# Optimization experiments

Hardware: AMD Instinct MI355X
Metric: run time of the kernel (lower is better)

Reference implementation:

```python
import jax, jax.numpy as jnp
import numpy as np

N_HEAD = 16
NUM_EXPERTS = 8
TOP_K = 2
LN_EPS = 1e-5


def setup_inputs() -> dict:
    key = jax.random.key(0)
    B, T, D = 8, 1024, 1024
    H = 4 * D
    E = NUM_EXPERTS
    ks = jax.random.split(key, 24)
    s = 0.02
    inp = {
        "x": jax.random.normal(ks[0], (B, T, D), jnp.float32),
        "ln1_g": jnp.ones((D,), jnp.float32),
        "ln1_b": jnp.zeros((D,), jnp.float32),
        "ln2_g": jnp.ones((D,), jnp.float32),
        "ln2_b": jnp.zeros((D,), jnp.float32),
        "Wq": jax.random.normal(ks[1], (D, D), jnp.float32) * s,
        "bq": jnp.zeros((D,), jnp.float32),
        "Wk": jax.random.normal(ks[2], (D, D), jnp.float32) * s,
        "bk": jnp.zeros((D,), jnp.float32),
        "Wv": jax.random.normal(ks[3], (D, D), jnp.float32) * s,
        "bv": jnp.zeros((D,), jnp.float32),
        "Wp": jax.random.normal(ks[4], (D, D), jnp.float32) * s,
        "bp": jnp.zeros((D,), jnp.float32),
        "gate_W": jax.random.normal(ks[5], (D, E), jnp.float32) * s,
        "gate_b": jnp.zeros((E,), jnp.float32),
        "exp_W1": jax.random.normal(ks[6], (E, D, H), jnp.float32) * s,
        "exp_b1": jnp.zeros((E, H), jnp.float32),
        "exp_W2": jax.random.normal(ks[7], (E, H, D), jnp.float32) * s,
        "exp_b2": jnp.zeros((E, D), jnp.float32),
    }
    return inp


def _layernorm(x, g, b):
    mu = jnp.mean(x, axis=-1, keepdims=True)
    var = jnp.mean(jnp.square(x - mu), axis=-1, keepdims=True)
    return (x - mu) * jax.lax.rsqrt(var + LN_EPS) * g + b


def _attention(h, Wq, bq, Wk, bk, Wv, bv, Wp, bp):
    B, T, D = h.shape
    hd = D // N_HEAD
    # [B,T,D] -> [B,Hh,T,hd]
    def split(z):
        return z.reshape(B, T, N_HEAD, hd).transpose(0, 2, 1, 3)
    q = split(h @ Wq + bq)
    k = split(h @ Wk + bk)
    v = split(h @ Wv + bv)
    att = jnp.einsum('bhqd,bhkd->bhqk', q, k) / jnp.sqrt(jnp.float32(hd))
    causal = jnp.tril(jnp.ones((T, T), bool))
    att = jnp.where(causal, att, -jnp.inf)
    att = jax.nn.softmax(att, axis=-1)
    y = jnp.einsum('bhqk,bhkd->bhqd', att, v)
    y = y.transpose(0, 2, 1, 3).reshape(B, T, D)
    return y @ Wp + bp


def _token_moe(h, gate_W, gate_b, exp_W1, exp_b1, exp_W2, exp_b2):
    B, T, D = h.shape
    flat = h.reshape(-1, D)                      # [N, D]
    N = flat.shape[0]
    logits = flat @ gate_W + gate_b              # [N, E]
    top_v, top_i = jax.lax.top_k(logits, TOP_K)  # [N, k]
    w = jax.nn.softmax(top_v, axis=-1)           # [N, k]
    # scatter top-k weights into dense [N, E] combine weights
    w_full = jnp.zeros((N, NUM_EXPERTS), flat.dtype)
    w_full = w_full.at[jnp.arange(N)[:, None], top_i].add(w)
    out = jnp.zeros_like(flat)
    for e in range(NUM_EXPERTS):  # small fixed expert count
        mid = jax.nn.gelu(flat @ exp_W1[e] + exp_b1[e], approximate=False)
        y_e = mid @ exp_W2[e] + exp_b2[e]
        out = out + w_full[:, e:e + 1] * y_e
    return out.reshape(B, T, D)


def reference(x, ln1_g, ln1_b, ln2_g, ln2_b, Wq, bq, Wk, bk, Wv, bv, Wp, bp,
              gate_W, gate_b, exp_W1, exp_b1, exp_W2, exp_b2):
    x = x + _attention(_layernorm(x, ln1_g, ln1_b), Wq, bq, Wk, bk, Wv, bv, Wp, bp)
    x = x + _token_moe(_layernorm(x, ln2_g, ln2_b), gate_W, gate_b,
                       exp_W1, exp_b1, exp_W2, exp_b2)
    return x
```

## Files before the change

kernel.cpp:

```cpp
#include <hip/hip_runtime.h>
#include <hip/hip_bf16.h>

#define D_MODEL 1024
#define H_MLP   4096
#define N_TOK   8192
#define T_SEQ   1024
#define NHEADS  16
#define HEAD_D  64
#define NEXPERT 8
#define LN_EPS  1e-5f
#define MAX_TILES 136
#define MAX_ROWS  (MAX_TILES * 128)
#define MB (1024 * 1024)

using f32x4 = __attribute__((ext_vector_type(4))) float;
using bh8   = __attribute__((ext_vector_type(8))) short;
typedef _Float16 h8 __attribute__((ext_vector_type(8)));

__device__ __forceinline__ unsigned short f2b(float f) {
  unsigned u = __float_as_uint(f);
  return (unsigned short)((u + 0x7FFFu + ((u >> 16) & 1u)) >> 16);
}
__device__ __forceinline__ float b2f(unsigned short h) {
  return __uint_as_float(((unsigned)h) << 16);
}
__device__ __forceinline__ void split16(float v, unsigned short& hi, unsigned short& lo) {
  const _Float16 h = (_Float16)v;
  const _Float16 l = (_Float16)(v - (float)h);
  hi = __builtin_bit_cast(unsigned short, h);
  lo = __builtin_bit_cast(unsigned short, l);
}
__device__ __forceinline__ void gll16(const unsigned short* g, unsigned short* lds) {
  __builtin_amdgcn_global_load_lds(
      (const __attribute__((address_space(1))) unsigned int*)(const void*)g,
      (__attribute__((address_space(3))) unsigned int*)(void*)lds, 16, 0, 0);
}

__global__ __launch_bounds__(256) void ln1_kernel(
    const float* __restrict__ x, const float* __restrict__ g,
    const float* __restrict__ b, unsigned short* __restrict__ oh,
    unsigned short* __restrict__ ol) {
  const int t = blockIdx.x, tid = threadIdx.x;
  const float4 v = ((const float4*)(x + (size_t)t * D_MODEL))[tid];
  float s  = v.x + v.y + v.z + v.w;
  float sq = v.x * v.x + v.y * v.y + v.z * v.z + v.w * v.w;
  __shared__ float red[8];
  #pragma unroll
  for (int o = 32; o > 0; o >>= 1) { s += __shfl_down(s, o); sq += __shfl_down(sq, o); }
  if ((tid & 63) == 0) { red[tid >> 6] = s; red[4 + (tid >> 6)] = sq; }
  __syncthreads();
  s  = red[0] + red[1] + red[2] + red[3];
  sq = red[4] + red[5] + red[6] + red[7];
  const float mu = s * (1.0f / D_MODEL);
  const float var = sq * (1.0f / D_MODEL) - mu * mu;
  const float rs = 1.0f / sqrtf(var + LN_EPS);
  const float4 gv = ((const float4*)g)[tid];
  const float4 bv = ((const float4*)b)[tid];
  float4 o;
  o.x = (v.x - mu) * rs * gv.x + bv.x;
  o.y = (v.y - mu) * rs * gv.y + bv.y;
  o.z = (v.z - mu) * rs * gv.z + bv.z;
  o.w = (v.w - mu) * rs * gv.w + bv.w;
  ushort4 hs, ls;
  split16(o.x, hs.x, ls.x); split16(o.y, hs.y, ls.y);
  split16(o.z, hs.z, ls.z); split16(o.w, hs.w, ls.w);
  ((ushort4*)(oh + (size_t)t * D_MODEL))[tid] = hs;
  ((ushort4*)(ol + (size_t)t * D_MODEL))[tid] = ls;
}

template<int MODE>
__global__ __launch_bounds__(256) void gemm_split_kernel(
    const unsigned short* __restrict__ Ah_g, const unsigned short* __restrict__ Al_g,
    const unsigned short* __restrict__ Bh_g, const unsigned short* __restrict__ Bl_g,
    const float* __restrict__ bias, const float* __restrict__ Rres,
    unsigned short* __restrict__ Ch, unsigned short* __restrict__ Cl,
    float* __restrict__ Cf, int M, int N, int K) {
  __shared__ unsigned short LAh[128 * 32], LAl[128 * 32];
  __shared__ unsigned short LBh[128 * 32], LBl[128 * 32];
  const int tid = threadIdx.x, lane = tid & 63, w = tid >> 6;
  const int bm = blockIdx.y * 128, bn = blockIdx.x * 128;
  const int wm = (w >> 1) * 64, wn = (w & 1) * 64;
  f32x4 acc[4][4];
  #pragma unroll
  for (int i = 0; i < 4; ++i)
    #pragma unroll
    for (int j = 0; j < 4; ++j) acc[i][j] = (f32x4){0.f, 0.f, 0.f, 0.f};
  const int lrow16 = lane >> 2, kq8 = (lane & 3) << 3;
  const int r0 = w * 16 + lrow16, r1 = 64 + w * 16 + lrow16;
  const size_t a0 = (size_t)(bm + r0) * K + kq8, a1 = (size_t)(bm + r1) * K + kq8;
  const size_t b0 = (size_t)(bn + r0) * K + kq8, b1 = (size_t)(bn + r1) * K + kq8;
  const int lb0 = (w * 16) * 32, lb1 = (64 + w * 16) * 32;
  const int lrow = lane & 15, lk = (lane >> 4) << 3;
  for (int k0 = 0; k0 < K; k0 += 32) {
    gll16(Ah_g + a0 + k0, &LAh[lb0]); gll16(Ah_g + a1 + k0, &LAh[lb1]);
    gll16(Al_g + a0 + k0, &LAl[lb0]); gll16(Al_g + a1 + k0, &LAl[lb1]);
    gll16(Bh_g + b0 + k0, &LBh[lb0]); gll16(Bh_g + b1 + k0, &LBh[lb1]);
    gll16(Bl_g + b0 + k0, &LBl[lb0]); gll16(Bl_g + b1 + k0, &LBl[lb1]);
    __syncthreads();
    h8 ah[4], al[4], bh[4], bl[4];
    #pragma unroll
    for (int i = 0; i < 4; ++i) {
      ah[i] = *(const h8*)&LAh[(wm + i * 16 + lrow) * 32 + lk];
      al[i] = *(const h8*)&LAl[(wm + i * 16 + lrow) * 32 + lk];
    }
    #pragma unroll
    for (int j = 0; j < 4; ++j) {
      bh[j] = *(const h8*)&LBh[(wn + j * 16 + lrow) * 32 + lk];
      bl[j] = *(const h8*)&LBl[(wn + j * 16 + lrow) * 32 + lk];
    }
    #pragma unroll
    for (int i = 0; i < 4; ++i)
      #pragma unroll
      for (int j = 0; j < 4; ++j) {
        acc[i][j] = __builtin_amdgcn_mfma_f32_16x16x32_f16(ah[i], bh[j], acc[i][j], 0, 0, 0);
        acc[i][j] = __builtin_amdgcn_mfma_f32_16x16x32_f16(ah[i], bl[j], acc[i][j], 0, 0, 0);
        acc[i][j] = __builtin_amdgcn_mfma_f32_16x16x32_f16(al[i], bh[j], acc[i][j], 0, 0, 0);
      }
    __syncthreads();
  }
  const int lc = lane & 15, lr4 = (lane >> 4) * 4;
  #pragma unroll
  for (int i = 0; i < 4; ++i)
    #pragma unroll
    for (int j = 0; j < 4; ++j) {
      const int col = bn + wn + j * 16 + lc;
      const float bsv = bias[col];
      #pragma unroll
      for (int qq = 0; qq < 4; ++qq) {
        const size_t row = (size_t)bm + wm + i * 16 + lr4 + qq;
        const size_t idx = row * N + col;
        const float v = acc[i][j][qq] + bsv;
        if (MODE == 0) {
          unsigned short hi, lo;
          split16(v, hi, lo);
          Ch[idx] = hi; Cl[idx] = lo;
        } else {
          Cf[idx] = v + Rres[idx];
        }
      }
    }
}

__global__ __launch_bounds__(256) void vtrans_kernel(
    const unsigned short* __restrict__ src, unsigned short* __restrict__ dst) {
  __shared__ unsigned short tile[64][72];
  const int tid = threadIdx.x;
  const int t0 = blockIdx.x * 64, bh = blockIdx.y;
  const int b = bh >> 4, h = bh & 15;
  #pragma unroll
  for (int it = 0; it < 2; ++it) {
    const int sg = tid + it * 256;
    const int r = sg >> 3, s = sg & 7;
    *(uint4*)&tile[r][s * 8] =
        *(const uint4*)(src + ((size_t)b * T_SEQ + t0 + r) * D_MODEL + h * HEAD_D + s * 8);
  }
  __syncthreads();
  #pragma unroll
  for (int it = 0; it < 2; ++it) {
    const int sg = tid + it * 256;
    const int d = sg >> 3, s = sg & 7;
    unsigned short v8[8] __attribute__((aligned(16)));
    #pragma unroll
    for (int j = 0; j < 8; ++j) v8[j] = tile[s * 8 + j][d];
    *(uint4*)(dst + ((size_t)bh * HEAD_D + d) * T_SEQ + t0 + s * 8) = *(const uint4*)v8;
  }
}

__global__ __launch_bounds__(512) void attn_mfma_kernel(
    const unsigned short* __restrict__ qh_g, const unsigned short* __restrict__ ql_g,
    const unsigned short* __restrict__ kh_g, const unsigned short* __restrict__ kl_g,
    const unsigned short* __restrict__ vth_g, const unsigned short* __restrict__ vtl_g,
    unsigned short* __restrict__ yh, unsigned short* __restrict__ yl) {
  __shared__ unsigned short Kh[64][72], Kl[64][72], Vh[64][72], Vl[64][72];
  __shared__ float Ps[8][16][36];
  const int tid = threadIdx.x, lane = tid & 63, w = tid >> 6;
  const int g = lane >> 4, c = lane & 15;
  const int qt = (int)gridDim.x - 1 - (int)blockIdx.x;
  const int bh = blockIdx.y, b = bh >> 4, h = bh & 15;
  const size_t qrow0 = (size_t)b * T_SEQ + qt * 128;
  h8 aqh[2], aql[2];
  {
    const size_t rq = (qrow0 + w * 16 + c) * D_MODEL + h * HEAD_D + g * 8;
    aqh[0] = *(const h8*)(qh_g + rq);
    aqh[1] = *(const h8*)(qh_g + rq + 32);
    aql[0] = *(const h8*)(ql_g + rq);
    aql[1] = *(const h8*)(ql_g + rq + 32);
  }
  f32x4 oacc[4];
  #pragma unroll
  for (int i = 0; i < 4; ++i) oacc[i] = (f32x4){0.f, 0.f, 0.f, 0.f};
  float m[4] = {-3e38f, -3e38f, -3e38f, -3e38f};
  float l[4] = {0.f, 0.f, 0.f, 0.f};
  const int sgr = tid >> 3, sgs = tid & 7;
  const int nkt = 2 * qt + 2;
  for (int kt = 0; kt < nkt; ++kt) {
    const int kv0 = kt * 64;
    __syncthreads();
    {
      const size_t kb = ((size_t)b * T_SEQ + kv0 + sgr) * D_MODEL + h * HEAD_D + sgs * 8;
      const size_t vb = ((size_t)bh * HEAD_D + sgr) * T_SEQ + kv0 + sgs * 8;
      *(uint4*)&Kh[sgr][sgs * 8] = *(const uint4*)(kh_g + kb);
      *(uint4*)&Kl[sgr][sgs * 8] = *(const uint4*)(kl_g + kb);
      *(uint4*)&Vh[sgr][sgs * 8] = *(const uint4*)(vth_g + vb);
      *(uint4*)&Vl[sgr][sgs * 8] = *(const uint4*)(vtl_g + vb);
    }
    __syncthreads();
    f32x4 sv[4];
    __builtin_amdgcn_s_setprio(1);
    #pragma unroll
    for (int nt = 0; nt < 4; ++nt) {
      f32x4 s = {0.f, 0.f, 0.f, 0.f};
      #pragma unroll
      for (int ks = 0; ks < 2; ++ks) {
        const h8 bkh = *(const h8*)&Kh[nt * 16 + c][ks * 32 + g * 8];
        const h8 bkl = *(const h8*)&Kl[nt * 16 + c][ks * 32 + g * 8];
        s = __builtin_amdgcn_mfma_f32_16x16x32_f16(aqh[ks], bkh, s, 0, 0, 0);
        s = __builtin_amdgcn_mfma_f32_16x16x32_f16(aqh[ks], bkl, s, 0, 0, 0);
        s = __builtin_amdgcn_mfma_f32_16x16x32_f16(aql[ks], bkh, s, 0, 0, 0);
      }
      sv[nt] = s;
    }
    __builtin_amdgcn_s_setprio(0);
    float pm[4] = {-3e38f, -3e38f, -3e38f, -3e38f};
    #pragma unroll
    for (int nt = 0; nt < 4; ++nt)
      #pragma unroll
      for (int qq = 0; qq < 4; ++qq) {
        float sval = sv[nt][qq] * 0.125f;
        const int krow = kv0 + nt * 16 + c;
        const int qrow = qt * 128 + w * 16 + g * 4 + qq;
        sval = (krow <= qrow) ? sval : -3.0e38f;
        sv[nt][qq] = sval;
        pm[qq] = fmaxf(pm[qq], sval);
      }
    #pragma unroll
    for (int o = 1; o < 16; o <<= 1)
      #pragma unroll
      for (int qq = 0; qq < 4; ++qq) pm[qq] = fmaxf(pm[qq], __shfl_xor(pm[qq], o));
    float psum[4];
    #pragma unroll
    for (int qq = 0; qq < 4; ++qq) {
      const float mnew = fmaxf(m[qq], pm[qq]);
      const float sc = expf(m[qq] - mnew);
      m[qq] = mnew;
      l[qq] *= sc;
      #pragma unroll
      for (int dt = 0; dt < 4; ++dt) oacc[dt][qq] *= sc;
      psum[qq] = 0.f;
    }
    #pragma unroll
    for (int nt = 0; nt < 4; ++nt)
      #pragma unroll
      for (int qq = 0; qq < 4; ++qq) {
        const float p = expf(sv[nt][qq] - m[qq]);
        sv[nt][qq] = p;
        psum[qq] += p;
      }
    #pragma unroll
    for (int o = 1; o < 16; o <<= 1)
      #pragma unroll
      for (int qq = 0; qq < 4; ++qq) psum[qq] += __shfl_xor(psum[qq], o);
    #pragma unroll
    for (int qq = 0; qq < 4; ++qq) l[qq] += psum[qq];
    #pragma unroll
    for (int half = 0; half < 2; ++half) {
      #pragma unroll
      for (int nt2 = 0; nt2 < 2; ++nt2)
        #pragma unroll
        for (int qq = 0; qq < 4; ++qq)
          Ps[w][g * 4 + qq][nt2 * 16 + c] = sv[half * 2 + nt2][qq];
      const float4 p0 = *(const float4*)&Ps[w][c][g * 8];
      const float4 p1 = *(const float4*)&Ps[w][c][g * 8 + 4];
      const float pv[8] = {p0.x, p0.y, p0.z, p0.w, p1.x, p1.y, p1.z, p1.w};
      h8 pah, pal;
      #pragma unroll
      for (int j = 0; j < 8; ++j) {
        const _Float16 hi = (_Float16)pv[j];
        pah[j] = hi;
        pal[j] = (_Float16)(pv[j] - (float)hi);
      }
      __builtin_amdgcn_s_setprio(1);
      #pragma unroll
      for (int dt = 0; dt < 4; ++dt) {
        const h8 bvh = *(const h8*)&Vh[dt * 16 + c][half * 32 + g * 8];
        const h8 bvl = *(const h8*)&Vl[dt * 16 + c][half * 32 + g * 8];
        oacc[dt] = __builtin_amdgcn_mfma_f32_16x16x32_f16(pah, bvh, oacc[dt], 0, 0, 0);
        oacc[dt] = __builtin_amdgcn_mfma_f32_16x16x32_f16(pah, bvl, oacc[dt], 0, 0, 0);
        oacc[dt] = __builtin_amdgcn_mfma_f32_16x16x32_f16(pal, bvh, oacc[dt], 0, 0, 0);
      }
      __builtin_amdgcn_s_setprio(0);
      if (half == 0) __builtin_amdgcn_sched_barrier(0);
    }
  }
  #pragma unroll
  for (int qq = 0; qq < 4; ++qq) {
    const float inv = 1.0f / l[qq];
    const size_t row = (qrow0 + w * 16 + g * 4 + qq) * D_MODEL + h * HEAD_D;
    #pragma unroll
    for (int dt = 0; dt < 4; ++dt) {
      unsigned short hi, lo;
      split16(oacc[dt][qq] * inv, hi, lo);
      yh[row + dt * 16 + c] = hi;
      yl[row + dt * 16 + c] = lo;
    }
  }
}

__global__ __launch_bounds__(256) void ln2_route_kernel(
    const float* __restrict__ x1, const float* __restrict__ g,
    const float* __restrict__ b, const float* __restrict__ gW,
    const float* __restrict__ gb, unsigned short* __restrict__ h2b,
    int2* __restrict__ tok_e, float2* __restrict__ tok_w, int* __restrict__ counts) {
  const int t = blockIdx.x, tid = threadIdx.x;
  const float4 v = ((const float4*)(x1 + (size_t)t * D_MODEL))[tid];
  float s  = v.x + v.y + v.z + v.w;
  float sq = v.x * v.x + v.y * v.y + v.z * v.z + v.w * v.w;
  __shared__ float red[8];
  __shared__ float lred[4][8];
  #pragma unroll
  for (int o = 32; o > 0; o >>= 1) { s += __shfl_down(s, o); sq += __shfl_down(sq, o); }
  if ((tid & 63) == 0) { red[tid >> 6] = s; red[4 + (tid >> 6)] = sq; }
  __syncthreads();
  s  = red[0] + red[1] + red[2] + red[3];
  sq = red[4] + red[5] + red[6] + red[7];
  const float mu = s * (1.0f / D_MODEL);
  const float var = sq * (1.0f / D_MODEL) - mu * mu;
  const float rs = 1.0f / sqrtf(var + LN_EPS);
  const float4 gv = ((const float4*)g)[tid];
  const float4 bv = ((const float4*)b)[tid];
  float4 hv;
  hv.x = (v.x - mu) * rs * gv.x + bv.x;
  hv.y = (v.y - mu) * rs * gv.y + bv.y;
  hv.z = (v.z - mu) * rs * gv.z + bv.z;
  hv.w = (v.w - mu) * rs * gv.w + bv.w;
  ushort4 hs;
  hs.x = f2b(hv.x); hs.y = f2b(hv.y); hs.z = f2b(hv.z); hs.w = f2b(hv.w);
  ((ushort4*)(h2b + (size_t)t * D_MODEL))[tid] = hs;
  float lg[8];
  const float* gwr = gW + (size_t)tid * 32;
  #pragma unroll
  for (int e = 0; e < 8; ++e)
    lg[e] = hv.x * gwr[e] + hv.y * gwr[8 + e] +
            hv.z * gwr[16 + e] + hv.w * gwr[24 + e];
  #pragma unroll
  for (int o = 32; o > 0; o >>= 1)
    #pragma unroll
    for (int e = 0; e < 8; ++e) lg[e] += __shfl_down(lg[e], o);
  if ((tid & 63) == 0)
    #pragma unroll
    for (int e = 0; e < 8; ++e) lred[tid >> 6][e] = lg[e];
  __syncthreads();
  if (tid == 0) {
    float L[8];
    #pragma unroll
    for (int e = 0; e < 8; ++e)
      L[e] = lred[0][e] + lred[1][e] + lred[2][e] + lred[3][e] + gb[e];
    int e0 = 0; float v0 = L[0];
    for (int e = 1; e < 8; ++e) if (L[e] > v0) { v0 = L[e]; e0 = e; }
    int e1 = (e0 == 0) ? 1 : 0; float v1 = L[e1];
    for (int e = 0; e < 8; ++e) if (e != e0 && L[e] > v1) { v1 = L[e]; e1 = e; }
    const float ew = expf(v1 - v0);
    const float inv = 1.0f / (1.0f + ew);
    tok_e[t] = make_int2(e0, e1);
    tok_w[t] = make_float2(inv, ew * inv);
    atomicAdd(&counts[e0], 1);
    atomicAdd(&counts[e1], 1);
  }
}

__global__ void route_offsets_kernel(const int* __restrict__ counts, int* __restrict__ off_al,
    int* __restrict__ ntiles, int* __restrict__ map_e, int* __restrict__ map_row) {
  if (threadIdx.x != 0 || blockIdx.x != 0) return;
  int off = 0, ti = 0;
  for (int e = 0; e < NEXPERT; ++e) {
    off_al[e] = off;
    const int tiles = (counts[e] + 127) >> 7;
    for (int j = 0; j < tiles; ++j) { map_e[ti] = e; map_row[ti] = off + (j << 7); ++ti; }
    off += tiles << 7;
  }
  off_al[NEXPERT] = off;
  ntiles[0] = ti;
}

__global__ __launch_bounds__(256) void place_kernel(
    const int2* __restrict__ tok_e, const int* __restrict__ off_al,
    int* __restrict__ cursors, int* __restrict__ list, int2* __restrict__ tok_pos) {
  const int t = blockIdx.x * 256 + threadIdx.x;
  if (t >= N_TOK) return;
  const int2 te = tok_e[t];
  const int p0 = off_al[te.x] + atomicAdd(&cursors[te.x], 1);
  const int p1 = off_al[te.y] + atomicAdd(&cursors[te.y], 1);
  list[p0] = t; list[p1] = t;
  tok_pos[t] = make_int2(p0, p1);
}

__global__ __launch_bounds__(256) void fill_pad_kernel(
    const int* __restrict__ counts, const int* __restrict__ off_al, int* __restrict__ list) {
  const int i = blockIdx.x * 256 + threadIdx.x;
  const int e = i >> 7, j = i & 127;
  if (e >= NEXPERT) return;
  const int start = off_al[e] + counts[e];
  if (start + j < off_al[e + 1]) list[start + j] = 0;
}

__global__ void transpose_cvt_kernel(
    const float* __restrict__ in, unsigned short* __restrict__ outp, int R, int C) {
  __shared__ float tile[32][33];
  const int e = blockIdx.z;
  const float* I = in + (size_t)e * R * C;
  unsigned short* O = outp + (size_t)e * R * C;
  const int c0 = blockIdx.x * 32, r0 = blockIdx.y * 32;
  const int tx = threadIdx.x, ty = threadIdx.y;
  #pragma unroll
  for (int j = 0; j < 32; j += 8)
    tile[ty + j][tx] = I[(size_t)(r0 + ty + j) * C + c0 + tx];
  __syncthreads();
  #pragma unroll
  for (int j = 0; j < 32; j += 8)
    O[(size_t)(c0 + ty + j) * R + r0 + tx] = f2b(tile[tx][ty + j]);
}

__global__ void transpose_cvt_f16_kernel(
    const float* __restrict__ in, unsigned short* __restrict__ oh,
    unsigned short* __restrict__ ol, int R, int C) {
  __shared__ float tile[32][33];
  const int c0 = blockIdx.x * 32, r0 = blockIdx.y * 32;
  const int tx = threadIdx.x, ty = threadIdx.y;
  #pragma unroll
  for (int j = 0; j < 32; j += 8)
    tile[ty + j][tx] = in[(size_t)(r0 + ty + j) * C + c0 + tx];
  __syncthreads();
  #pragma unroll
  for (int j = 0; j < 32; j += 8) {
    unsigned short hi, lo;
    split16(tile[tx][ty + j], hi, lo);
    oh[(size_t)(c0 + ty + j) * R + r0 + tx] = hi;
    ol[(size_t)(c0 + ty + j) * R + r0 + tx] = lo;
  }
}

template<int GELU_OUT, int GATHER>
__global__ __launch_bounds__(256) void moe_gemm_kernel(
    const unsigned short* __restrict__ Abase, const unsigned short* __restrict__ Bbase,
    const float* __restrict__ biasBase, unsigned short* __restrict__ midOut,
    float* __restrict__ fOut, const int* __restrict__ list,
    const int* __restrict__ map_e, const int* __restrict__ map_row,
    const int* __restrict__ ntiles_p, int K, int N) {
  const int mt = blockIdx.y;
  if (mt >= ntiles_p[0]) return;
  const int e = map_e[mt];
  const int row0 = map_row[mt];
  const int bn = blockIdx.x * 128;
  const unsigned short* Bp = Bbase + (size_t)e * (size_t)N * (size_t)K;
  const float* bias = biasBase + (size_t)e * N;
  __shared__ unsigned short As[128 * 32];
  __shared__ unsigned short Bs[128 * 32];
  const int tid = threadIdx.x, lane = tid & 63, wid = tid >> 6;
  const int wm = (wid >> 1) * 64, wn = (wid & 1) * 64;
  f32x4 acc[4][4];
  #pragma unroll
  for (int i = 0; i < 4; ++i)
    #pragma unroll
    for (int j = 0; j < 4; ++j) acc[i][j] = (f32x4){0.f, 0.f, 0.f, 0.f};
  const int lrow16 = lane >> 2, kq8 = (lane & 3) << 3;
  const int r0 = wid * 16 + lrow16, r1 = 64 + wid * 16 + lrow16;
  size_t arow0, arow1;
  if (GATHER) {
    arow0 = (size_t)list[row0 + r0] * (size_t)K + kq8;
    arow1 = (size_t)list[row0 + r1] * (size_t)K + kq8;
  } else {
    arow0 = (size_t)(row0 + r0) * (size_t)K + kq8;
    arow1 = (size_t)(row0 + r1) * (size_t)K + kq8;
  }
  const size_t brow0 = (size_t)(bn + r0) * (size_t)K + kq8;
  const size_t brow1 = (size_t)(bn + r1) * (size_t)K + kq8;
  const int lb0 = (wid * 16) * 32, lb1 = (64 + wid * 16) * 32;
  const int lrow = lane & 15, lk = (lane >> 4) << 3;
  for (int k0 = 0; k0 < K; k0 += 32) {
    gll16(Abase + arow0 + k0, &As[lb0]);
    gll16(Abase + arow1 + k0, &As[lb1]);
    gll16(Bp + brow0 + k0, &Bs[lb0]);
    gll16(Bp + brow1 + k0, &Bs[lb1]);
    __syncthreads();
    bh8 a[4], b[4];
    #pragma unroll
    for (int i = 0; i < 4; ++i) a[i] = *(const bh8*)&As[(wm + i * 16 + lrow) * 32 + lk];
    #pragma unroll
    for (int j = 0; j < 4; ++j) b[j] = *(const bh8*)&Bs[(wn + j * 16 + lrow) * 32 + lk];
    #pragma unroll
    for (int i = 0; i < 4; ++i)
      #pragma unroll
      for (int j = 0; j < 4; ++j)
        acc[i][j] = __builtin_amdgcn_mfma_f32_16x16x32_bf16(a[i], b[j], acc[i][j], 0, 0, 0);
    __syncthreads();
  }
  const int lc = lane & 15, lr4 = (lane >> 4) * 4;
  #pragma unroll
  for (int i = 0; i < 4; ++i)
    #pragma unroll
    for (int j = 0; j < 4; ++j) {
      const int col = bn + wn + j * 16 + lc;
      const float bsv = bias[col];
      #pragma unroll
      for (int qq = 0; qq < 4; ++qq) {
        const int rowl = wm + i * 16 + lr4 + qq;
        const size_t idx = (size_t)(row0 + rowl) * N + col;
        const float xv = acc[i][j][qq] + bsv;
        if (GELU_OUT) {
          const float gel = 0.5f * xv * (1.0f + erff(xv * 0.70710678118654752f));
          midOut[idx] = f2b(gel);
        } else {
          fOut[idx] = xv;
        }
      }
    }
}

__global__ __launch_bounds__(256) void combine_kernel(
    const float* __restrict__ x1, const float* __restrict__ ylist,
    const int2* __restrict__ tok_pos, const float2* __restrict__ tok_w,
    float* __restrict__ outp) {
  const int t = blockIdx.x, tid = threadIdx.x;
  const int2 p = tok_pos[t];
  const float2 w = tok_w[t];
  const float4 a  = ((const float4*)(x1 + (size_t)t * D_MODEL))[tid];
  const float4 y0 = ((const float4*)(ylist + (size_t)p.x * D_MODEL))[tid];
  const float4 y1 = ((const float4*)(ylist + (size_t)p.y * D_MODEL))[tid];
  float4 o;
  o.x = a.x + w.x * y0.x + w.y * y1.x;
  o.y = a.y + w.x * y0.y + w.y * y1.y;
  o.z = a.z + w.x * y0.z + w.y * y1.z;
  o.w = a.w + w.x * y0.w + w.y * y1.w;
  ((float4*)(outp + (size_t)t * D_MODEL))[tid] = o;
}

extern "C" void kernel_launch(void* const* d_in, const int* in_sizes, int n_in,
                              void* d_out, int out_size, void* d_ws, size_t ws_size,
                              hipStream_t stream) {
  const float* x    = (const float*)d_in[0];
  const float* ln1g = (const float*)d_in[1];
  const float* ln1b = (const float*)d_in[2];
  const float* ln2g = (const float*)d_in[3];
  const float* ln2b = (const float*)d_in[4];
  const float* Wq   = (const float*)d_in[5];
  const float* bq   = (const float*)d_in[6];
  const float* Wk   = (const float*)d_in[7];
  const float* bk   = (const float*)d_in[8];
  const float* Wv   = (const float*)d_in[9];
  const float* bv   = (const float*)d_in[10];
  const float* Wp   = (const float*)d_in[11];
  const float* bp   = (const float*)d_in[12];
  const float* gW   = (const float*)d_in[13];
  const float* gb   = (const float*)d_in[14];
  const float* eW1  = (const float*)d_in[15];
  const float* eb1  = (const float*)d_in[16];
  const float* eW2  = (const float*)d_in[17];
  const float* eb2  = (const float*)d_in[18];
  float* out = (float*)d_out;
  (void)in_sizes; (void)n_in; (void)out_size;

  char* wsb = (char*)d_ws;
  size_t off = 0;
  auto alloc = [&](size_t bytes) -> void* {
    void* p = wsb + off;
    off += (bytes + 255) & ~(size_t)255;
    return p;
  };
  int*  counts  = (int*)alloc(32);
  int*  cursors = (int*)alloc(32);
  int*  off_al  = (int*)alloc(64);
  int*  ntiles  = (int*)alloc(64);
  int*  map_e   = (int*)alloc(MAX_TILES * 4);
  int*  map_row = (int*)alloc(MAX_TILES * 4);
  const size_t ctrl_bytes = off;
  int2*   tok_e   = (int2*)alloc((size_t)N_TOK * 8);
  float2* tok_w   = (float2*)alloc((size_t)N_TOK * 8);
  int2*   tok_pos = (int2*)alloc((size_t)N_TOK * 8);
  int*    list    = (int*)alloc((size_t)MAX_ROWS * 4);
  float* x1  = (float*)alloc((size_t)N_TOK * D_MODEL * 4);
  unsigned short* h2b = (unsigned short*)alloc((size_t)N_TOK * D_MODEL * 2);
  unsigned short* W1T = (unsigned short*)alloc((size_t)NEXPERT * D_MODEL * H_MLP * 2);
  unsigned short* W2T = (unsigned short*)alloc((size_t)NEXPERT * D_MODEL * H_MLP * 2);
  float* ylist = (float*)alloc((size_t)MAX_ROWS * D_MODEL * 4);
  unsigned short* WqTh = (unsigned short*)alloc((size_t)D_MODEL * D_MODEL * 2);
  unsigned short* WqTl = (unsigned short*)alloc((size_t)D_MODEL * D_MODEL * 2);
  unsigned short* WkTh = (unsigned short*)alloc((size_t)D_MODEL * D_MODEL * 2);
  unsigned short* WkTl = (unsigned short*)alloc((size_t)D_MODEL * D_MODEL * 2);
  unsigned short* WvTh = (unsigned short*)alloc((size_t)D_MODEL * D_MODEL * 2);
  unsigned short* WvTl = (unsigned short*)alloc((size_t)D_MODEL * D_MODEL * 2);
  unsigned short* WpTh = (unsigned short*)alloc((size_t)D_MODEL * D_MODEL * 2);
  unsigned short* WpTl = (unsigned short*)alloc((size_t)D_MODEL * D_MODEL * 2);
  char* arena = (char*)alloc((size_t)160 * MB);
  unsigned short* h1h = (unsigned short*)(arena);
  unsigned short* h1l = (unsigned short*)(arena + (size_t) 16 * MB);
  unsigned short* qh_ = (unsigned short*)(arena + (size_t) 32 * MB);
  unsigned short* ql_ = (unsigned short*)(arena + (size_t) 48 * MB);
  unsigned short* kh_ = (unsigned short*)(arena + (size_t) 64 * MB);
  unsigned short* kl_ = (unsigned short*)(arena + (size_t) 80 * MB);
  unsigned short* vh_ = (unsigned short*)(arena + (size_t) 96 * MB);
  unsigned short* vl_ = (unsigned short*)(arena + (size_t)112 * MB);
  unsigned short* vth_ = (unsigned short*)(arena + (size_t)128 * MB);
  unsigned short* vtl_ = (unsigned short*)(arena + (size_t)144 * MB);
  unsigned short* yh_ = vh_;
  unsigned short* yl_ = vl_;
  unsigned short* mid = (unsigned short*)(arena);
  if (off > ws_size) return;

  hipMemsetAsync(d_ws, 0, ctrl_bytes, stream);

  transpose_cvt_kernel<<<dim3(H_MLP / 32, D_MODEL / 32, NEXPERT), dim3(32, 8), 0, stream>>>(
      eW1, W1T, D_MODEL, H_MLP);
  transpose_cvt_kernel<<<dim3(D_MODEL / 32, H_MLP / 32, NEXPERT), dim3(32, 8), 0, stream>>>(
      eW2, W2T, H_MLP, D_MODEL);
  transpose_cvt_f16_kernel<<<dim3(32, 32), dim3(32, 8), 0, stream>>>(Wq, WqTh, WqTl, D_MODEL, D_MODEL);
  transpose_cvt_f16_kernel<<<dim3(32, 32), dim3(32, 8), 0, stream>>>(Wk, WkTh, WkTl, D_MODEL, D_MODEL);
  transpose_cvt_f16_kernel<<<dim3(32, 32), dim3(32, 8), 0, stream>>>(Wv, WvTh, WvTl, D_MODEL, D_MODEL);
  transpose_cvt_f16_kernel<<<dim3(32, 32), dim3(32, 8), 0, stream>>>(Wp, WpTh, WpTl, D_MODEL, D_MODEL);

  ln1_kernel<<<N_TOK, 256, 0, stream>>>(x, ln1g, ln1b, h1h, h1l);

  gemm_split_kernel<0><<<dim3(8, 64), 256, 0, stream>>>(
      h1h, h1l, WqTh, WqTl, bq, nullptr, qh_, ql_, nullptr, N_TOK, D_MODEL, D_MODEL);
  gemm_split_kernel<0><<<dim3(8, 64), 256, 0, stream>>>(
      h1h, h1l, WkTh, WkTl, bk, nullptr, kh_, kl_, nullptr, N_TOK, D_MODEL, D_MODEL);
  gemm_split_kernel<0><<<dim3(8, 64), 256, 0, stream>>>(
      h1h, h1l, WvTh, WvTl, bv, nullptr, vh_, vl_, nullptr, N_TOK, D_MODEL, D_MODEL);

  vtrans_kernel<<<dim3(T_SEQ / 64, (N_TOK / T_SEQ) * NHEADS), 256, 0, stream>>>(vh_, vth_);
  vtrans_kernel<<<dim3(T_SEQ / 64, (N_TOK / T_SEQ) * NHEADS), 256, 0, stream>>>(vl_, vtl_);

  attn_mfma_kernel<<<dim3(T_SEQ / 128, (N_TOK / T_SEQ) * NHEADS), 512, 0, stream>>>(
      qh_, ql_, kh_, kl_, vth_, vtl_, yh_, yl_);

  gemm_split_kernel<1><<<dim3(8, 64), 256, 0, stream>>>(
      yh_, yl_, WpTh, WpTl, bp, x, nullptr, nullptr, x1, N_TOK, D_MODEL, D_MODEL);

  ln2_route_kernel<<<N_TOK, 256, 0, stream>>>(x1, ln2g, ln2b, gW, gb, h2b, tok_e, tok_w, counts);
  route_offsets_kernel<<<1, 64, 0, stream>>>(counts, off_al, ntiles, map_e, map_row);
  place_kernel<<<N_TOK / 256, 256, 0, stream>>>(tok_e, off_al, cursors, list, tok_pos);
  fill_pad_kernel<<<4, 256, 0, stream>>>(counts, off_al, list);

  moe_gemm_kernel<1, 1><<<dim3(H_MLP / 128, MAX_TILES), 256, 0, stream>>>(
      h2b, W1T, eb1, mid, nullptr, list, map_e, map_row, ntiles, D_MODEL, H_MLP);
  moe_gemm_kernel<0, 0><<<dim3(D_MODEL / 128, MAX_TILES), 256, 0, stream>>>(
      mid, W2T, eb2, nullptr, ylist, list, map_e, map_row, ntiles, H_MLP, D_MODEL);

  combine_kernel<<<N_TOK, 256, 0, stream>>>(x1, ylist, tok_pos, tok_w, out);
}
```

Baseline: 1.325 ms.

## Double-buffer LDS in MoE expert GEMM with async prefetch two tiles ahead

The MoE expert GEMM now keeps two LDS buffers for the A and B tiles and issues direct-to-LDS global loads for tile t+2 while tile t is being consumed. Explicit vmcnt waits and raw barriers replace the two __syncthreads per k-step, so global load latency can overlap MFMA work. It also raises wave priority around the MFMA block via s_setprio. This doubles LDS use per block, which may lower occupancy, and relies on hand-placed waitcnt values being correct.

```diff
diff --git a/kernel.cpp b/kernel.cpp
--- a/kernel.cpp
+++ b/kernel.cpp
@@ -453,8 +453,8 @@
   const int bn = blockIdx.x * 128;
   const unsigned short* Bp = Bbase + (size_t)e * (size_t)N * (size_t)K;
   const float* bias = biasBase + (size_t)e * N;
-  __shared__ unsigned short As[128 * 32];
-  __shared__ unsigned short Bs[128 * 32];
+  __shared__ unsigned short As[2 * 128 * 32];
+  __shared__ unsigned short Bs[2 * 128 * 32];
   const int tid = threadIdx.x, lane = tid & 63, wid = tid >> 6;
   const int wm = (wid >> 1) * 64, wn = (wid & 1) * 64;
   f32x4 acc[4][4];
@@ -476,23 +476,50 @@
   const size_t brow1 = (size_t)(bn + r1) * (size_t)K + kq8;
   const int lb0 = (wid * 16) * 32, lb1 = (64 + wid * 16) * 32;
   const int lrow = lane & 15, lk = (lane >> 4) << 3;
-  for (int k0 = 0; k0 < K; k0 += 32) {
-    gll16(Abase + arow0 + k0, &As[lb0]);
-    gll16(Abase + arow1 + k0, &As[lb1]);
-    gll16(Bp + brow0 + k0, &Bs[lb0]);
-    gll16(Bp + brow1 + k0, &Bs[lb1]);
-    __syncthreads();
+  const int NT = K >> 5;
+  gll16(Abase + arow0, &As[lb0]);
+  gll16(Abase + arow1, &As[lb1]);
+  gll16(Bp + brow0, &Bs[lb0]);
+  gll16(Bp + brow1, &Bs[lb1]);
+  __builtin_amdgcn_sched_barrier(0);
+  gll16(Abase + arow0 + 32, &As[4096 + lb0]);
+  gll16(Abase + arow1 + 32, &As[4096 + lb1]);
+  gll16(Bp + brow0 + 32, &Bs[4096 + lb0]);
+  gll16(Bp + brow1 + 32, &Bs[4096 + lb1]);
+  asm volatile("s_waitcnt vmcnt(4)" ::: "memory");
+  __builtin_amdgcn_sched_barrier(0);
+  __builtin_amdgcn_s_barrier();
+  __builtin_amdgcn_sched_barrier(0);
+  for (int t = 0; t < NT; ++t) {
+    const int boff = (t & 1) << 12;
     bh8 a[4], b[4];
     #pragma unroll
-    for (int i = 0; i < 4; ++i) a[i] = *(const bh8*)&As[(wm + i * 16 + lrow) * 32 + lk];
-    #pragma unroll
-    for (int j = 0; j < 4; ++j) b[j] = *(const bh8*)&Bs[(wn + j * 16 + lrow) * 32 + lk];
+    for (int i = 0; i < 4; ++i) a[i] = *(const bh8*)&As[boff + (wm + i * 16 + lrow) * 32 + lk];
+    #pragma unroll
+    for (int j = 0; j < 4; ++j) b[j] = *(const bh8*)&Bs[boff + (wn + j * 16 + lrow) * 32 + lk];
+    __builtin_amdgcn_s_setprio(1);
     #pragma unroll
     for (int i = 0; i < 4; ++i)
       #pragma unroll
       for (int j = 0; j < 4; ++j)
         acc[i][j] = __builtin_amdgcn_mfma_f32_16x16x32_bf16(a[i], b[j], acc[i][j], 0, 0, 0);
-    __syncthreads();
+    __builtin_amdgcn_s_setprio(0);
+    __builtin_amdgcn_sched_barrier(0);
+    __builtin_amdgcn_s_barrier();
+    __builtin_amdgcn_sched_barrier(0);
+    if (t + 2 < NT) {
+      const size_t k2 = (size_t)(t + 2) << 5;
+      gll16(Abase + arow0 + k2, &As[boff + lb0]);
+      gll16(Abase + arow1 + k2, &As[boff + lb1]);
+      gll16(Bp + brow0 + k2, &Bs[boff + lb0]);
+      gll16(Bp + brow1 + k2, &Bs[boff + lb1]);
+      asm volatile("s_waitcnt vmcnt(4)" ::: "memory");
+    } else {
+      asm volatile("s_waitcnt vmcnt(0)" ::: "memory");
+    }
+    __builtin_amdgcn_sched_barrier(0);
+    __builtin_amdgcn_s_barrier();
+    __builtin_amdgcn_sched_barrier(0);
   }
   const int lc = lane & 15, lr4 = (lane >> 4) * 4;
   #pragma unroll
```

Result: slower. 1.377 ms (+3.9%).
